# Optimization experiments

Hardware: AMD Instinct MI355X
Metric: run time of the kernel (lower is better)

Reference implementation:

```python
import jax, jax.numpy as jnp
import numpy as np

B, S, E = 2, 4096, 1024
H = 16
W = 256  # attention_window == chunk size; attn width = 3*W


def _chunk3(x):
    # x: [b, nc, w, h, d] -> stack (prev, cur, next) chunks on last axis: [b, nc, w, h, d, 3]
    prev = jnp.pad(x[:, :-1], ((0, 0), (1, 0), (0, 0), (0, 0), (0, 0)))
    nxt = jnp.pad(x[:, 1:], ((0, 0), (0, 1), (0, 0), (0, 0), (0, 0)))
    return jnp.stack([prev, x, nxt], axis=-1)


def setup_inputs() -> dict:
    key = jax.random.key(0)
    ks = jax.random.split(key, 4)
    hs = jax.random.normal(ks[0], (B, S, E), jnp.float32)

    def lin(k):
        kw, kb = jax.random.split(k)
        return (jax.random.normal(kw, (E, E), jnp.float32) * 0.02,
                jax.random.normal(kb, (E,), jnp.float32) * 0.02)

    Wq, bq = lin(ks[1])
    Wk, bk = lin(ks[2])
    Wv, bv = lin(ks[3])
    return {"hidden_states": hs, "Wq": Wq, "bq": bq, "Wk": Wk, "bk": bk, "Wv": Wv, "bv": bv}


def reference(hidden_states, Wq, bq, Wk, bk, Wv, bv):
    b, s, e = hidden_states.shape
    h, w = H, W
    d = e // h
    nc = s // w  # number of non-overlapping chunks

    # torch nn.Linear: y = x @ W.T + b ; q scaled by 1/sqrt(head_dim)
    q = (hidden_states @ Wq.T + bq) * (1.0 / np.sqrt(d))
    k = hidden_states @ Wk.T + bk
    v = hidden_states @ Wv.T + bv
    q = q.reshape(b, s, h, d)
    k = k.reshape(b, s, h, d)
    v = v.reshape(b, s, h, d)

    # ---- sliding_chunks_no_overlap_matmul_qk ----
    cq = q.reshape(b, nc, w, h, d)
    ck3 = _chunk3(k.reshape(b, nc, w, h, d))  # [b,nc,w,h,d,3]
    # [b,nc,w,h,3,w] -> [b,s,h,3w]
    scores = jnp.einsum('bcxhd,bcyhde->bcxhey', cq, ck3).reshape(b, s, h, 3 * w)

    # ---- mask_invalid_locations (same math as Longformer's helper) ----
    ii = jnp.arange(w)[:, None]
    cc = jnp.arange(w + 1)[None, :]
    beg_mask = cc < (w - ii)   # [w, w+1] applied to first w rows, first w+1 cols
    end_mask = cc >= (w - ii)  # flipped mask, last w rows, last w+1 cols
    neg_inf = jnp.array(-jnp.inf, scores.dtype)
    beg = jnp.where(beg_mask[None, :, None, :], neg_inf, scores[:, :w, :, :w + 1])
    scores = scores.at[:, :w, :, :w + 1].set(beg)
    end = jnp.where(end_mask[None, :, None, :], neg_inf, scores[:, s - w:, :, 3 * w - (w + 1):])
    scores = scores.at[:, s - w:, :, 3 * w - (w + 1):].set(end)

    # softmax in float32 (as in original), cast back
    probs = jax.nn.softmax(scores.astype(jnp.float32), axis=-1).astype(hidden_states.dtype)

    # ---- sliding_chunks_no_overlap_matmul_pv ----
    cp = probs.reshape(b, nc, w, h, 3, w)          # bcwhpd (d = key pos in chunk)
    cv3 = _chunk3(v.reshape(b, nc, w, h, d))       # bcdhep (d = pos, e = head_dim, p = 3)
    attn = jnp.einsum('bcwhpd,bcdhep->bcwhe', cp, cv3).reshape(b, s, h, d)

    return attn.reshape(b, s, e)
```

## Files before the change

### kernel.cpp

```cpp
#include <hip/hip_runtime.h>
#include <math.h>

#define BB  2
#define SS  4096
#define EE  1024
#define HH  16
#define DD  64
#define WW  256
#define NCC 16
#define MTOT (BB*SS)

typedef __attribute__((ext_vector_type(4))) float f32x4;
typedef __attribute__((ext_vector_type(8))) short bf16x8;

__device__ __forceinline__ void gl_lds16(const void* g, void* l) {
  __builtin_amdgcn_global_load_lds(
      (const __attribute__((address_space(1))) unsigned int*)g,
      (__attribute__((address_space(3))) unsigned int*)l,
      16, 0, 0);
}

__device__ __forceinline__ unsigned bf16rne(float f) {
  unsigned u = __float_as_uint(f);
  return (u + (((u >> 16) & 1u) + 0x7fffu)) >> 16;
}

__device__ __forceinline__ unsigned long long pack64(unsigned a, unsigned b,
                                                     unsigned c2, unsigned d) {
  return (unsigned long long)(a | (b << 16)) |
         ((unsigned long long)(c2 | (d << 16)) << 32);
}

__global__ __launch_bounds__(256) void split_all(
    const float* __restrict__ hs, const float* __restrict__ Wq,
    const float* __restrict__ Wk, const float* __restrict__ Wv,
    unsigned short* __restrict__ Ahi, unsigned short* __restrict__ Alo,
    unsigned short* __restrict__ Wqh, unsigned short* __restrict__ Wql,
    unsigned short* __restrict__ Wkh, unsigned short* __restrict__ Wkl,
    unsigned short* __restrict__ Wvh, unsigned short* __restrict__ Wvl)
{
  const int bx = blockIdx.x;
  const float* src; unsigned short *hi, *lo; size_t blk;
  if (bx < 8192)       { src = hs; hi = Ahi; lo = Alo; blk = bx; }
  else if (bx < 9216)  { src = Wq; hi = Wqh; lo = Wql; blk = bx - 8192; }
  else if (bx < 10240) { src = Wk; hi = Wkh; lo = Wkl; blk = bx - 9216; }
  else                 { src = Wv; hi = Wvh; lo = Wvl; blk = bx - 10240; }

  const size_t i = blk * 256 + threadIdx.x;
  const float4 v = ((const float4*)src)[i];
  float f[4] = {v.x, v.y, v.z, v.w};
  unsigned short h[4], l[4];
  #pragma unroll
  for (int j = 0; j < 4; ++j) {
    unsigned u  = __float_as_uint(f[j]);
    unsigned uh = u & 0xFFFF0000u;
    h[j] = (unsigned short)(uh >> 16);
    float r = f[j] - __uint_as_float(uh);
    unsigned ur = __float_as_uint(r);
    ur += ((ur >> 16) & 1u) + 0x7FFFu;
    l[j] = (unsigned short)(ur >> 16);
  }
  *(ushort4*)&hi[4*i] = make_ushort4(h[0], h[1], h[2], h[3]);
  *(ushort4*)&lo[4*i] = make_ushort4(l[0], l[1], l[2], l[3]);
}

struct ProjArgs {
  const unsigned short* Wh;
  const unsigned short* Wl;
  const float* bias;
  unsigned short* outHi;
  unsigned short* outLo;
  float scale;
};

__global__ __launch_bounds__(512) void mfma_proj(
    const unsigned short* __restrict__ Ahi,
    const unsigned short* __restrict__ Alo,
    ProjArgs p0, ProjArgs p1, ProjArgs p2)
{
  __shared__ __align__(16) union {
    unsigned short stage[3][24576];
    unsigned short ep[128][136];
  } sh;

  const int tid  = threadIdx.x;
  const int lane = tid & 63;
  const int wid  = tid >> 6;
  const int wr   = wid >> 1;
  const int wc   = wid & 1;
  const int m0   = blockIdx.x * 256, n0 = blockIdx.y * 128;
  const ProjArgs P = (blockIdx.z == 0) ? p0 : ((blockIdx.z == 1) ? p1 : p2);

  const int qA0 = tid, qA1 = 512 + tid;
  const int rowA0 = ((qA0 >> 5) << 3) | (qA0 & 7), kcA0 = (qA0 >> 3) & 3;
  const int rowA1 = ((qA1 >> 5) << 3) | (qA1 & 7), kcA1 = (qA1 >> 3) & 3;
  const int rowB  = rowA0, kcB = kcA0;

  const size_t aoff0 = (size_t)(m0 + rowA0) * 2048 + (size_t)(kcA0 * 16);
  const size_t aoff1 = (size_t)(m0 + rowA1) * 2048 + (size_t)(kcA1 * 16);
  const size_t boff  = (size_t)(n0 + rowB)  * 2048 + (size_t)(kcB  * 16);

  const int dstA0 = wid * 1024;
  const int dstA1 = 8192 + wid * 1024;
  const int dstB  = wid * 1024;

  const char* gAh = (const char*)Ahi;
  const char* gAl = (const char*)Alo;
  const char* gBh = (const char*)P.Wh;
  const char* gBl = (const char*)P.Wl;

  const int fr = lane & 15;
  const int kc = lane >> 4;
  int a_o[4], b_o[4];
  #pragma unroll
  for (int f = 0; f < 4; ++f) {
    int r = wr * 64 + f * 16 + fr;
    a_o[f] = ((r >> 3) << 9) | (kc << 7) | ((r & 7) << 4);
    r = wc * 64 + f * 16 + fr;
    b_o[f] = ((r >> 3) << 9) | (kc << 7) | ((r & 7) << 4);
  }

  f32x4 acc[4][4];
  #pragma unroll
  for (int i = 0; i < 4; ++i)
    #pragma unroll
    for (int j = 0; j < 4; ++j) acc[i][j] = (f32x4){0.f, 0.f, 0.f, 0.f};

  char* const Lp = (char*)&sh.stage[0][0];
  #define PL(b, p) (Lp + ((b) * 49152 + (p)))

  #define STAGE(buf, ks) { const size_t kb = (size_t)(ks) * 64; \
    gl_lds16(gAh + aoff0 + kb, PL(buf,0)     + dstA0); \
    gl_lds16(gAh + aoff1 + kb, PL(buf,0)     + dstA1); \
    gl_lds16(gAl + aoff0 + kb, PL(buf,16384) + dstA0); \
    gl_lds16(gAl + aoff1 + kb, PL(buf,16384) + dstA1); \
    gl_lds16(gBh + boff  + kb, PL(buf,32768) + dstB); \
    gl_lds16(gBl + boff  + kb, PL(buf,40960) + dstB); }

  bf16x8 ah0[4], bh0[4], ah1[4], bh1[4];
  bf16x8 al[4], bl[4];

  #define RD_C1(AH, BH, buf) { \
    _Pragma("unroll") \
    for (int f = 0; f < 4; ++f) { \
      AH[f] = *(const bf16x8*)(PL(buf,0)     + a_o[f]); \
      BH[f] = *(const bf16x8*)(PL(buf,32768) + b_o[f]); \
    } }
  #define RD_C2(buf) { \
    _Pragma("unroll") \
    for (int f = 0; f < 4; ++f) { \
      al[f] = *(const bf16x8*)(PL(buf,16384) + a_o[f]); \
      bl[f] = *(const bf16x8*)(PL(buf,40960) + b_o[f]); \
    } }

  #define MM16(AA, BBV) { \
    _Pragma("unroll") \
    for (int i = 0; i < 4; ++i) \
      _Pragma("unroll") \
      for (int j = 0; j < 4; ++j) \
        acc[i][j] = __builtin_amdgcn_mfma_f32_16x16x32_bf16(AA[i], BBV[j], acc[i][j], 0,0,0); }

  #define ITER(KS, B, BN, AHc, BHc, AHn, BHn, VM, DOSTAGE, DONEXT) { \
    RD_C2(B); \
    __builtin_amdgcn_sched_barrier(0); \
    asm volatile("s_waitcnt lgkmcnt(8)" ::: "memory"); \
    __builtin_amdgcn_sched_barrier(0); \
    __builtin_amdgcn_s_setprio(1); \
    MM16(AHc, BHc); \
    __builtin_amdgcn_s_setprio(0); \
    __builtin_amdgcn_sched_barrier(0); \
    asm volatile("s_waitcnt lgkmcnt(0)" ::: "memory"); \
    __builtin_amdgcn_sched_barrier(0); \
    __builtin_amdgcn_s_barrier(); \
    if (DOSTAGE) STAGE(B, (KS)+3); \
    if (VM == 12)     { asm volatile("s_waitcnt vmcnt(12)" ::: "memory"); } \
    else if (VM == 6) { asm volatile("s_waitcnt vmcnt(6)"  ::: "memory"); } \
    else if (VM == 0) { asm volatile("s_waitcnt vmcnt(0)"  ::: "memory"); } \
    if (VM >= 0) { __builtin_amdgcn_sched_barrier(0); __builtin_amdgcn_s_barrier(); } \
    if (DONEXT) RD_C1(AHn, BHn, BN); \
    __builtin_amdgcn_s_setprio(1); \
    MM16(AHc, bl); \
    MM16(al, BHc); \
    __builtin_amdgcn_s_setprio(0); \
  }

  STAGE(0, 0);
  STAGE(1, 1);
  STAGE(2, 2);
  asm volatile("s_waitcnt vmcnt(12)" ::: "memory");
  __builtin_amdgcn_sched_barrier(0);
  __builtin_amdgcn_s_barrier();
  RD_C1(ah0, bh0, 0);

  for (int kk = 0; kk < 24; kk += 6) {
    ITER(kk+0, 0, 1, ah0, bh0, ah1, bh1, 12, 1, 1);
    ITER(kk+1, 1, 2, ah1, bh1, ah0, bh0, 12, 1, 1);
    ITER(kk+2, 2, 0, ah0, bh0, ah1, bh1, 12, 1, 1);
    ITER(kk+3, 0, 1, ah1, bh1, ah0, bh0, 12, 1, 1);
    ITER(kk+4, 1, 2, ah0, bh0, ah1, bh1, 12, 1, 1);
    ITER(kk+5, 2, 0, ah1, bh1, ah0, bh0, 12, 1, 1);
  }
  ITER(24, 0, 1, ah0, bh0, ah1, bh1, 12, 1, 1);
  ITER(25, 1, 2, ah1, bh1, ah0, bh0, 12, 1, 1);
  ITER(26, 2, 0, ah0, bh0, ah1, bh1, 12, 1, 1);
  ITER(27, 0, 1, ah1, bh1, ah0, bh0, 12, 1, 1);
  ITER(28, 1, 2, ah0, bh0, ah1, bh1, 12, 1, 1);
  ITER(29, 2, 0, ah1, bh1, ah0, bh0,  6, 0, 1);
  ITER(30, 0, 1, ah0, bh0, ah1, bh1,  0, 0, 1);
  ITER(31, 1, 2, ah1, bh1, ah0, bh0, -1, 0, 0);
  #undef PL
  #undef STAGE
  #undef RD_C1
  #undef RD_C2
  #undef MM16
  #undef ITER

  const int r4 = (lane >> 4) << 2;
  #pragma unroll
  for (int hh = 0; hh < 2; ++hh) {
    #pragma unroll
    for (int plane = 0; plane < 2; ++plane) {
      __syncthreads();
      if ((wr >> 1) == hh) {
        #pragma unroll
        for (int j = 0; j < 4; ++j) {
          const int col_l = wc*64 + j*16 + fr;
          const float bv = P.bias[n0 + col_l];
          #pragma unroll
          for (int i = 0; i < 4; ++i) {
            const int rl0 = (wr & 1)*64 + i*16 + r4;
            #pragma unroll
            for (int v = 0; v < 4; ++v) {
              const float val = (acc[i][j][v] + bv) * P.scale;
              const unsigned u = __float_as_uint(val);
              unsigned sv;
              if (plane == 0) { sv = u >> 16; }
              else {
                const float rres = val - __uint_as_float(u & 0xFFFF0000u);
                unsigned ur = __float_as_uint(rres);
                ur += ((ur >> 16) & 1u) + 0x7FFFu; sv = ur >> 16;
              }
              const int rl = rl0 + v;
              sh.ep[rl][(((col_l >> 3) ^ (rl & 7)) << 3) + (col_l & 7)] =
                  (unsigned short)sv;
            }
          }
        }
      }
      __syncthreads();
      unsigned short* const OUT = plane ? P.outLo : P.outHi;
      #pragma unroll
      for (int u2 = 0; u2 < 4; ++u2) {
        const int chunk = u2 * 512 + tid;
        const int rr = chunk >> 4, c16 = chunk & 15;
        const bf16x8 vv = *(const bf16x8*)&sh.ep[rr][(c16 ^ (rr & 7)) << 3];
        *(bf16x8*)&OUT[(size_t)(m0 + hh*128 + rr) * EE + n0 + c16*8] = vv;
      }
    }
  }
}

__global__ __launch_bounds__(256) void attn_mfma(
    const unsigned short* __restrict__ Qh_g, const unsigned short* __restrict__ Ql_g,
    const unsigned short* __restrict__ Kh_g, const unsigned short* __restrict__ Kl_g,
    const unsigned short* __restrict__ Vh_g, const unsigned short* __restrict__ Vl_g,
    float* __restrict__ Og)
{
  __shared__ __align__(16) unsigned short Kf[2][2048];
  __shared__ __align__(16) unsigned short Vt[2][2048];
  __shared__ unsigned long long Pscr[4][256];

  const int c = blockIdx.x, h = blockIdx.y, bz = blockIdx.z;
  const int b = bz >> 1, qh = bz & 1;
  const int tid = threadIdx.x;
  const int lane = tid & 63, wid = tid >> 6;
  const int g = lane >> 4, lq = lane & 15;

  const size_t chunk0 = (size_t)(b * NCC + c) * WW;
  const size_t qrow0  = chunk0 + (size_t)qh * 128;
  const int colh = h * DD;

  bf16x8 qfh[2][2], qfl[2][2];
  #pragma unroll
  for (int s = 0; s < 2; ++s)
    #pragma unroll
    for (int ch = 0; ch < 2; ++ch) {
      const size_t off = (qrow0 + wid*32 + s*16 + lq) * EE + colh + ch*32 + g*8;
      qfh[s][ch] = *(const bf16x8*)(Qh_g + off);
      qfl[s][ch] = *(const bf16x8*)(Ql_g + off);
    }

  f32x4 Oa[4][2];
  #pragma unroll
  for (int i = 0; i < 4; ++i)
    #pragma unroll
    for (int j = 0; j < 2; ++j) Oa[i][j] = (f32x4){0.f, 0.f, 0.f, 0.f};
  float m[2], lsum[2];
  #pragma unroll
  for (int s = 0; s < 2; ++s) { m[s] = -1e30f; lsum[s] = 0.f; }

  const int kK = 16*(wid & 1) + lq;
  const int dK = 32*(wid >> 1) + g*8;
  const int stv = tid >> 5, idxv = tid & 31;
  const int kV = 16*(stv >> 2) + (idxv >> 1);
  const int dV = 16*(stv & 3) + 8*(idxv & 1);
  const int C0  = ((dV >> 4) << 6) | ((kV >> 3) << 4) | (dV & 15);
  const int swW = (((dV >> 4) & 1) << 2) | (((kV >> 3) & 1) << 1) | ((dV >> 3) & 1);
  const int vel = kV & 7;

  const long krow0_base = (long)chunk0 - WW;
  const int t0 = (c == 0) ? 8 : 0;
  const int tN = (c == NCC-1) ? 16 : 24;

  uint4 rkh, rkl, rvh, rvl;
  {
    const long kr = krow0_base + (long)t0*32;
    const size_t offK = (size_t)(kr + kK) * EE + colh + dK;
    const size_t offV = (size_t)(kr + kV) * EE + colh + dV;
    rkh = *(const uint4*)(Kh_g + offK); rkl = *(const uint4*)(Kl_g + offK);
    rvh = *(const uint4*)(Vh_g + offV); rvl = *(const uint4*)(Vl_g + offV);
  }

  for (int tt = t0; tt < tN; ++tt) {
    __syncthreads();
    *(uint4*)&Kf[0][wid*512 + lane*8] = rkh;
    *(uint4*)&Kf[1][wid*512 + lane*8] = rkl;
    {
      const unsigned hw[4] = {rvh.x, rvh.y, rvh.z, rvh.w};
      const unsigned lw[4] = {rvl.x, rvl.y, rvl.z, rvl.w};
      #pragma unroll
      for (int t = 0; t < 8; ++t) {
        const int ii = C0*8 + ((t ^ swW) << 3) + vel;
        Vt[0][ii] = (unsigned short)(hw[t >> 1] >> ((t & 1) * 16));
        Vt[1][ii] = (unsigned short)(lw[t >> 1] >> ((t & 1) * 16));
      }
    }
    __syncthreads();

    if (tt + 1 < tN) {
      const long kr = krow0_base + (long)(tt+1)*32;
      const size_t offK = (size_t)(kr + kK) * EE + colh + dK;
      const size_t offV = (size_t)(kr + kV) * EE + colh + dV;
      rkh = *(const uint4*)(Kh_g + offK); rkl = *(const uint4*)(Kl_g + offK);
      rvh = *(const uint4*)(Vh_g + offV); rvl = *(const uint4*)(Vl_g + offV);
    }

    bf16x8 kfh[2][2], kfl[2][2];
    #pragma unroll
    for (int f = 0; f < 4; ++f) {
      const int o = f*512 + lane*8;
      kfh[f & 1][f >> 1] = *(const bf16x8*)&Kf[0][o];
      kfl[f & 1][f >> 1] = *(const bf16x8*)&Kf[1][o];
    }

    bf16x8 vfh[4], vfl[4];
    #pragma unroll
    for (int ds = 0; ds < 4; ++ds) {
      const int rch = ds*64 + g*16 + lq;
      const int rsw = (((rch >> 6) & 1) << 2) | (((rch >> 4) & 1) << 1) | ((rch >> 3) & 1);
      vfh[ds] = *(const bf16x8*)&Vt[0][(rch ^ rsw) * 8];
      vfl[ds] = *(const bf16x8*)&Vt[1][(rch ^ rsw) * 8];
    }

    #pragma unroll
    for (int s = 0; s < 2; ++s) {
      f32x4 ac0 = (f32x4){0.f,0.f,0.f,0.f}, ac1 = (f32x4){0.f,0.f,0.f,0.f};
      #pragma unroll
      for (int ch = 0; ch < 2; ++ch) {
        ac0 = __builtin_amdgcn_mfma_f32_16x16x32_bf16(kfh[0][ch], qfh[s][ch], ac0, 0,0,0);
        ac0 = __builtin_amdgcn_mfma_f32_16x16x32_bf16(kfh[0][ch], qfl[s][ch], ac0, 0,0,0);
        ac0 = __builtin_amdgcn_mfma_f32_16x16x32_bf16(kfl[0][ch], qfh[s][ch], ac0, 0,0,0);
        ac1 = __builtin_amdgcn_mfma_f32_16x16x32_bf16(kfh[1][ch], qfh[s][ch], ac1, 0,0,0);
        ac1 = __builtin_amdgcn_mfma_f32_16x16x32_bf16(kfh[1][ch], qfl[s][ch], ac1, 0,0,0);
        ac1 = __builtin_amdgcn_mfma_f32_16x16x32_bf16(kfl[1][ch], qfh[s][ch], ac1, 0,0,0);
      }

      float tmax = fmaxf(fmaxf(fmaxf(ac0[0],ac0[1]), fmaxf(ac0[2],ac0[3])),
                         fmaxf(fmaxf(ac1[0],ac1[1]), fmaxf(ac1[2],ac1[3])));
      tmax = fmaxf(tmax, __shfl_xor(tmax, 16));
      tmax = fmaxf(tmax, __shfl_xor(tmax, 32));
      const float mo = m[s];
      const float mn = fmaxf(mo, tmax);
      m[s] = mn;
      const float sc = __expf(mo - mn);
      float pv[8];
      #pragma unroll
      for (int r = 0; r < 4; ++r) { pv[r] = __expf(ac0[r] - mn); pv[4+r] = __expf(ac1[r] - mn); }
      float ps = 0.f;
      #pragma unroll
      for (int r = 0; r < 8; ++r) ps += pv[r];
      lsum[s] = lsum[s] * sc + ps;
      #pragma unroll
      for (int ds = 0; ds < 4; ++ds) Oa[ds][s] *= sc;

      unsigned hb[8], lb[8];
      #pragma unroll
      for (int r = 0; r < 8; ++r) {
        hb[r] = bf16rne(pv[r]);
        const float rr = pv[r] - __uint_as_float(hb[r] << 16);
        lb[r] = bf16rne(rr);
      }
      const int pq = (g >> 1)*32 + lq*2 + (g & 1);
      Pscr[wid][pq]            = pack64(hb[0],hb[1],hb[2],hb[3]);
      Pscr[wid][pq + 64]       = pack64(hb[4],hb[5],hb[6],hb[7]);
      Pscr[wid][128 + pq]      = pack64(lb[0],lb[1],lb[2],lb[3]);
      Pscr[wid][128 + pq + 64] = pack64(lb[4],lb[5],lb[6],lb[7]);
      asm volatile("" ::: "memory");
      union U8 { unsigned long long q[2]; bf16x8 v; };
      U8 uh, ul;
      uh.q[0] = Pscr[wid][lane*2];       uh.q[1] = Pscr[wid][lane*2 + 1];
      ul.q[0] = Pscr[wid][128 + lane*2]; ul.q[1] = Pscr[wid][128 + lane*2 + 1];
      const bf16x8 pbh = uh.v;
      const bf16x8 pbl = ul.v;

      #pragma unroll
      for (int ds = 0; ds < 4; ++ds) {
        Oa[ds][s] = __builtin_amdgcn_mfma_f32_16x16x32_bf16(vfh[ds], pbh, Oa[ds][s], 0,0,0);
        Oa[ds][s] = __builtin_amdgcn_mfma_f32_16x16x32_bf16(vfl[ds], pbh, Oa[ds][s], 0,0,0);
        Oa[ds][s] = __builtin_amdgcn_mfma_f32_16x16x32_bf16(vfh[ds], pbl, Oa[ds][s], 0,0,0);
      }
    }
  }

  #pragma unroll
  for (int s = 0; s < 2; ++s) {
    float ls = lsum[s];
    ls += __shfl_xor(ls, 16);
    ls += __shfl_xor(ls, 32);
    const int x = qh*128 + wid*32 + s*16 + lq;
    const float nz = (c == 0) ? (float)x
                   : ((c == NCC-1) ? (float)(WW - 1 - x) : 0.f);
    ls += nz * __expf(0.f - m[s]);
    const float inv = 1.f / ls;
    float* op = Og + (chunk0 + x) * EE + colh;
    #pragma unroll
    for (int ds = 0; ds < 4; ++ds) {
      float4 r;
      r.x = Oa[ds][s][0]*inv; r.y = Oa[ds][s][1]*inv;
      r.z = Oa[ds][s][2]*inv; r.w = Oa[ds][s][3]*inv;
      *(float4*)(op + ds*16 + g*4) = r;
    }
  }
}

extern "C" void kernel_launch(void* const* d_in, const int* in_sizes, int n_in,
                              void* d_out, int out_size, void* d_ws, size_t ws_size,
                              hipStream_t stream) {
    const float* hs = (const float*)d_in[0];
    const float* Wq = (const float*)d_in[1];
    const float* bq = (const float*)d_in[2];
    const float* Wk = (const float*)d_in[3];
    const float* bk = (const float*)d_in[4];
    const float* Wv = (const float*)d_in[5];
    const float* bv = (const float*)d_in[6];
    float* out = (float*)d_out;

    const size_t mat  = (size_t)MTOT * EE;
    const size_t wmat = (size_t)EE * EE;

    unsigned short* w = (unsigned short*)d_ws;
    unsigned short* Ahi = w;            unsigned short* Alo = Ahi + mat;
    unsigned short* Wqh = Alo + mat;    unsigned short* Wql = Wqh + wmat;
    unsigned short* Wkh = Wql + wmat;   unsigned short* Wkl = Wkh + wmat;
    unsigned short* Wvh = Wkl + wmat;   unsigned short* Wvl = Wvh + wmat;
    unsigned short* Qhb = Wvl + wmat;   unsigned short* Qlb = Qhb + mat;
    unsigned short* Khb = Qlb + mat;    unsigned short* Klb = Khb + mat;
    unsigned short* Vhb = Klb + mat;    unsigned short* Vlb = Vhb + mat;

    split_all<<<8192 + 3*1024, 256, 0, stream>>>(
        hs, Wq, Wk, Wv, Ahi, Alo, Wqh, Wql, Wkh, Wkl, Wvh, Wvl);

    ProjArgs pq{Wqh, Wql, bq, Qhb, Qlb, 0.125f};
    ProjArgs pk{Wkh, Wkl, bk, Khb, Klb, 1.0f};
    ProjArgs pv{Wvh, Wvl, bv, Vhb, Vlb, 1.0f};
    dim3 g(MTOT/256, EE/128, 3);
    mfma_proj<<<g, 512, 0, stream>>>(Ahi, Alo, pq, pk, pv);

    dim3 ga(NCC, HH, BB*2);
    attn_mfma<<<ga, 256, 0, stream>>>(Qhb, Qlb, Khb, Klb, Vhb, Vlb, out);
}
```

Measured before the change: 299.5 us.

## Load projection weight fragments directly from global into registers, bypassing LDS

The B operand (weight hi/lo planes) of the split-bf16 projection GEMM is now read straight from global memory into MFMA register fragments one k-step ahead, instead of being staged through LDS. This shrinks the LDS stage buffers from 48KB to 32KB per stage and removes B LDS reads, with the vmcnt/lgkmcnt waits reworked around the extra in-flight global loads. The risk is that each wave issues uncoalesced global loads of weights with little cross-wave reuse, adding L2 traffic and latency exposure while raising register pressure.

```diff
diff --git a/kernel.cpp b/kernel.cpp
--- a/kernel.cpp
+++ b/kernel.cpp
@@ -79,7 +79,7 @@
     ProjArgs p0, ProjArgs p1, ProjArgs p2)
 {
   __shared__ __align__(16) union {
-    unsigned short stage[3][24576];
+    unsigned short stage[3][16384];
     unsigned short ep[128][136];
   } sh;
 
@@ -94,30 +94,27 @@
   const int qA0 = tid, qA1 = 512 + tid;
   const int rowA0 = ((qA0 >> 5) << 3) | (qA0 & 7), kcA0 = (qA0 >> 3) & 3;
   const int rowA1 = ((qA1 >> 5) << 3) | (qA1 & 7), kcA1 = (qA1 >> 3) & 3;
-  const int rowB  = rowA0, kcB = kcA0;
 
   const size_t aoff0 = (size_t)(m0 + rowA0) * 2048 + (size_t)(kcA0 * 16);
   const size_t aoff1 = (size_t)(m0 + rowA1) * 2048 + (size_t)(kcA1 * 16);
-  const size_t boff  = (size_t)(n0 + rowB)  * 2048 + (size_t)(kcB  * 16);
 
   const int dstA0 = wid * 1024;
   const int dstA1 = 8192 + wid * 1024;
-  const int dstB  = wid * 1024;
 
   const char* gAh = (const char*)Ahi;
   const char* gAl = (const char*)Alo;
-  const char* gBh = (const char*)P.Wh;
-  const char* gBl = (const char*)P.Wl;
+  const unsigned short* gBh16 = P.Wh;
+  const unsigned short* gBl16 = P.Wl;
 
   const int fr = lane & 15;
   const int kc = lane >> 4;
-  int a_o[4], b_o[4];
+  int a_o[4];
+  unsigned b_go[4];
   #pragma unroll
   for (int f = 0; f < 4; ++f) {
     int r = wr * 64 + f * 16 + fr;
     a_o[f] = ((r >> 3) << 9) | (kc << 7) | ((r & 7) << 4);
-    r = wc * 64 + f * 16 + fr;
-    b_o[f] = ((r >> 3) << 9) | (kc << 7) | ((r & 7) << 4);
+    b_go[f] = (unsigned)((n0 + wc * 64 + f * 16 + fr) * EE + kc * 8);
   }
 
   f32x4 acc[4][4];
@@ -127,31 +124,33 @@
     for (int j = 0; j < 4; ++j) acc[i][j] = (f32x4){0.f, 0.f, 0.f, 0.f};
 
   char* const Lp = (char*)&sh.stage[0][0];
-  #define PL(b, p) (Lp + ((b) * 49152 + (p)))
+  #define PL(b, p) (Lp + ((b) * 32768 + (p)))
 
   #define STAGE(buf, ks) { const size_t kb = (size_t)(ks) * 64; \
     gl_lds16(gAh + aoff0 + kb, PL(buf,0)     + dstA0); \
     gl_lds16(gAh + aoff1 + kb, PL(buf,0)     + dstA1); \
     gl_lds16(gAl + aoff0 + kb, PL(buf,16384) + dstA0); \
-    gl_lds16(gAl + aoff1 + kb, PL(buf,16384) + dstA1); \
-    gl_lds16(gBh + boff  + kb, PL(buf,32768) + dstB); \
-    gl_lds16(gBl + boff  + kb, PL(buf,40960) + dstB); }
-
-  bf16x8 ah0[4], bh0[4], ah1[4], bh1[4];
-  bf16x8 al[4], bl[4];
-
-  #define RD_C1(AH, BH, buf) { \
+    gl_lds16(gAl + aoff1 + kb, PL(buf,16384) + dstA1); }
+
+  #define LOADB(BH, BL, ks) { \
     _Pragma("unroll") \
     for (int f = 0; f < 4; ++f) { \
-      AH[f] = *(const bf16x8*)(PL(buf,0)     + a_o[f]); \
-      BH[f] = *(const bf16x8*)(PL(buf,32768) + b_o[f]); \
+      BH[f] = *(const bf16x8*)(gBh16 + b_go[f] + (unsigned)((ks) * 32)); \
+      BL[f] = *(const bf16x8*)(gBl16 + b_go[f] + (unsigned)((ks) * 32)); \
     } }
+
+  bf16x8 ah0[4], ah1[4];
+  bf16x8 al[4];
+  bf16x8 b0h[4], b0l[4], b1h[4], b1l[4];
+
+  #define RD_C1(AH, buf) { \
+    _Pragma("unroll") \
+    for (int f = 0; f < 4; ++f) \
+      AH[f] = *(const bf16x8*)(PL(buf,0) + a_o[f]); }
   #define RD_C2(buf) { \
     _Pragma("unroll") \
-    for (int f = 0; f < 4; ++f) { \
-      al[f] = *(const bf16x8*)(PL(buf,16384) + a_o[f]); \
-      bl[f] = *(const bf16x8*)(PL(buf,40960) + b_o[f]); \
-    } }
+    for (int f = 0; f < 4; ++f) \
+      al[f] = *(const bf16x8*)(PL(buf,16384) + a_o[f]); }
 
   #define MM16(AA, BBV) { \
     _Pragma("unroll") \
@@ -160,56 +159,60 @@
       for (int j = 0; j < 4; ++j) \
         acc[i][j] = __builtin_amdgcn_mfma_f32_16x16x32_bf16(AA[i], BBV[j], acc[i][j], 0,0,0); }
 
-  #define ITER(KS, B, BN, AHc, BHc, AHn, BHn, VM, DOSTAGE, DONEXT) { \
+  #define ITER(KS, B, BN, AHc, AHn, BHc, BLc, BHn, BLn, VM, DOSTAGE, DOLOADB, DONEXT) { \
     RD_C2(B); \
+    if (DOLOADB) LOADB(BHn, BLn, (KS)+1); \
     __builtin_amdgcn_sched_barrier(0); \
-    asm volatile("s_waitcnt lgkmcnt(8)" ::: "memory"); \
+    asm volatile("s_waitcnt lgkmcnt(4)" ::: "memory");    \
     __builtin_amdgcn_sched_barrier(0); \
     __builtin_amdgcn_s_setprio(1); \
-    MM16(AHc, BHc); \
+    MM16(AHc, BHc);                                       \
     __builtin_amdgcn_s_setprio(0); \
     __builtin_amdgcn_sched_barrier(0); \
-    asm volatile("s_waitcnt lgkmcnt(0)" ::: "memory"); \
+    asm volatile("s_waitcnt lgkmcnt(0)" ::: "memory");    \
     __builtin_amdgcn_sched_barrier(0); \
-    __builtin_amdgcn_s_barrier(); \
+    __builtin_amdgcn_s_barrier();                         \
     if (DOSTAGE) STAGE(B, (KS)+3); \
-    if (VM == 12)     { asm volatile("s_waitcnt vmcnt(12)" ::: "memory"); } \
-    else if (VM == 6) { asm volatile("s_waitcnt vmcnt(6)"  ::: "memory"); } \
-    else if (VM == 0) { asm volatile("s_waitcnt vmcnt(0)"  ::: "memory"); } \
+    if (VM == 20)      { asm volatile("s_waitcnt vmcnt(20)" ::: "memory"); } \
+    else if (VM == 16) { asm volatile("s_waitcnt vmcnt(16)" ::: "memory"); } \
+    else if (VM == 12) { asm volatile("s_waitcnt vmcnt(12)" ::: "memory"); } \
+    else if (VM == 0)  { asm volatile("s_waitcnt vmcnt(0)"  ::: "memory"); } \
     if (VM >= 0) { __builtin_amdgcn_sched_barrier(0); __builtin_amdgcn_s_barrier(); } \
-    if (DONEXT) RD_C1(AHn, BHn, BN); \
+    if (DONEXT) RD_C1(AHn, BN); \
     __builtin_amdgcn_s_setprio(1); \
-    MM16(AHc, bl); \
-    MM16(al, BHc); \
+    MM16(AHc, BLc);                                       \
+    MM16(al, BHc);                                        \
     __builtin_amdgcn_s_setprio(0); \
   }
 
   STAGE(0, 0);
+  LOADB(b0h, b0l, 0);
   STAGE(1, 1);
   STAGE(2, 2);
-  asm volatile("s_waitcnt vmcnt(12)" ::: "memory");
+  asm volatile("s_waitcnt vmcnt(8)" ::: "memory");
   __builtin_amdgcn_sched_barrier(0);
   __builtin_amdgcn_s_barrier();
-  RD_C1(ah0, bh0, 0);
-
-  for (int kk = 0; kk < 24; kk += 6) {
-    ITER(kk+0, 0, 1, ah0, bh0, ah1, bh1, 12, 1, 1);
-    ITER(kk+1, 1, 2, ah1, bh1, ah0, bh0, 12, 1, 1);
-    ITER(kk+2, 2, 0, ah0, bh0, ah1, bh1, 12, 1, 1);
-    ITER(kk+3, 0, 1, ah1, bh1, ah0, bh0, 12, 1, 1);
-    ITER(kk+4, 1, 2, ah0, bh0, ah1, bh1, 12, 1, 1);
-    ITER(kk+5, 2, 0, ah1, bh1, ah0, bh0, 12, 1, 1);
-  }
-  ITER(24, 0, 1, ah0, bh0, ah1, bh1, 12, 1, 1);
-  ITER(25, 1, 2, ah1, bh1, ah0, bh0, 12, 1, 1);
-  ITER(26, 2, 0, ah0, bh0, ah1, bh1, 12, 1, 1);
-  ITER(27, 0, 1, ah1, bh1, ah0, bh0, 12, 1, 1);
-  ITER(28, 1, 2, ah0, bh0, ah1, bh1, 12, 1, 1);
-  ITER(29, 2, 0, ah1, bh1, ah0, bh0,  6, 0, 1);
-  ITER(30, 0, 1, ah0, bh0, ah1, bh1,  0, 0, 1);
-  ITER(31, 1, 2, ah1, bh1, ah0, bh0, -1, 0, 0);
+  RD_C1(ah0, 0);
+
+  ITER(0, 0, 1, ah0, ah1, b0h, b0l, b1h, b1l, 12, 1, 1, 1);
+  ITER(1, 1, 2, ah1, ah0, b1h, b1l, b0h, b0l, 20, 1, 1, 1);
+  for (int kk = 2; kk < 26; kk += 6) {
+    ITER(kk+0, 2, 0, ah0, ah1, b0h, b0l, b1h, b1l, 20, 1, 1, 1);
+    ITER(kk+1, 0, 1, ah1, ah0, b1h, b1l, b0h, b0l, 20, 1, 1, 1);
+    ITER(kk+2, 1, 2, ah0, ah1, b0h, b0l, b1h, b1l, 20, 1, 1, 1);
+    ITER(kk+3, 2, 0, ah1, ah0, b1h, b1l, b0h, b0l, 20, 1, 1, 1);
+    ITER(kk+4, 0, 1, ah0, ah1, b0h, b0l, b1h, b1l, 20, 1, 1, 1);
+    ITER(kk+5, 1, 2, ah1, ah0, b1h, b1l, b0h, b0l, 20, 1, 1, 1);
+  }
+  ITER(26, 2, 0, ah0, ah1, b0h, b0l, b1h, b1l, 20, 1, 1, 1);
+  ITER(27, 0, 1, ah1, ah0, b1h, b1l, b0h, b0l, 20, 1, 1, 1);
+  ITER(28, 1, 2, ah0, ah1, b0h, b0l, b1h, b1l, 20, 1, 1, 1);
+  ITER(29, 2, 0, ah1, ah0, b1h, b1l, b0h, b0l, 20, 0, 1, 1);
+  ITER(30, 0, 1, ah0, ah1, b0h, b0l, b1h, b1l, 16, 0, 1, 1);
+  ITER(31, 1, 2, ah1, ah0, b1h, b1l, b0h, b0l, -1, 0, 0, 0);
   #undef PL
   #undef STAGE
+  #undef LOADB
   #undef RD_C1
   #undef RD_C2
   #undef MM16
```

New measurement: 419.2 us. 39.9% more time.
